# Performance work log

Hardware: AMD Instinct MI355X
Metric: run time of the kernel (lower is better)

Reference implementation:

```python
import jax, jax.numpy as jnp
import numpy as np
import math

D_MODEL = 512
NUM_HEADS = 8
D_HEAD = D_MODEL // NUM_HEADS
B, S = 4, 2048
L = 2 * S - 1  # relative position range


def _rel_shift(pos_score):
    # pos_score: [B, H, S, L] -> [B, H, S, L//2+1] via pad/reshape/slice trick
    b, h, s, l = pos_score.shape
    padded = jnp.pad(pos_score, ((0, 0), (0, 0), (0, 0), (1, 0)))  # [B,H,S,L+1]
    padded = padded.reshape(b, h, l + 1, s)
    shifted = padded[:, :, 1:].reshape(b, h, s, l)
    return shifted[..., : l // 2 + 1]


def setup_inputs() -> dict:
    key = jax.random.key(0)
    ks = jax.random.split(key, 16)
    std = 1.0 / math.sqrt(D_MODEL)
    inp = {
        "query": jax.random.normal(ks[0], (B, S, D_MODEL), jnp.float32),
        "key": jax.random.normal(ks[1], (B, S, D_MODEL), jnp.float32),
        "value": jax.random.normal(ks[2], (B, S, D_MODEL), jnp.float32),
        "pos_embedding": jax.random.normal(ks[3], (B, L, D_MODEL), jnp.float32),
        "Wq": jax.random.normal(ks[4], (D_MODEL, D_MODEL), jnp.float32) * std,
        "bq": jnp.zeros((D_MODEL,), jnp.float32),
        "Wk": jax.random.normal(ks[5], (D_MODEL, D_MODEL), jnp.float32) * std,
        "bk": jnp.zeros((D_MODEL,), jnp.float32),
        "Wv": jax.random.normal(ks[6], (D_MODEL, D_MODEL), jnp.float32) * std,
        "bv": jnp.zeros((D_MODEL,), jnp.float32),
        "Wp": jax.random.normal(ks[7], (D_MODEL, D_MODEL), jnp.float32) * std,
        "u_bias": jax.random.normal(ks[8], (NUM_HEADS, D_HEAD), jnp.float32) * std,
        "v_bias": jax.random.normal(ks[9], (NUM_HEADS, D_HEAD), jnp.float32) * std,
        "Wo": jax.random.normal(ks[10], (D_MODEL, D_MODEL), jnp.float32) * std,
        "bo": jnp.zeros((D_MODEL,), jnp.float32),
    }
    return inp


def reference(query, key, value, pos_embedding, Wq, bq, Wk, bk, Wv, bv, Wp, u_bias, v_bias, Wo, bo):
    b, s, d = query.shape
    h, dh = u_bias.shape
    sqrt_dim = jnp.asarray(math.sqrt(d), query.dtype)

    q = (query @ Wq.T + bq).reshape(b, s, h, dh)
    k = (key @ Wk.T + bk).reshape(b, -1, h, dh)
    v = (value @ Wv.T + bv).reshape(b, -1, h, dh)
    p = (pos_embedding @ Wp.T).reshape(b, -1, h, dh)

    content_score = jnp.einsum("bshd,bthd->bhst", q + u_bias, k)
    pos_score = jnp.einsum("bshd,blhd->bhsl", q + v_bias, p)
    pos_score = _rel_shift(pos_score)  # [B,H,S,S]

    score = (content_score + pos_score) / sqrt_dim
    attn = jax.nn.softmax(score, axis=-1)
    context = jnp.einsum("bhst,bthd->bshd", attn, v).reshape(b, s, d)
    return context @ Wo.T + bo
```

## Files before the change

kernel.cpp:

```cpp
#include <hip/hip_runtime.h>


typedef __bf16 bf16;
typedef __bf16 bf16x4 __attribute__((ext_vector_type(4)));
typedef __bf16 bf16x8 __attribute__((ext_vector_type(8)));
typedef float  f32x4  __attribute__((ext_vector_type(4)));

#define MFMA(A,B,C) __builtin_amdgcn_mfma_f32_16x16x32_bf16((A),(B),(C),0,0,0)

constexpr float SCP = 1.44269504088896f / 22.6274169979695f;

__device__ __forceinline__ void gload16(const void* g, void* l) {
    __builtin_amdgcn_global_load_lds(
        (const __attribute__((address_space(1))) void*)g,
        (__attribute__((address_space(3))) void*)l, 16, 0, 0);
}

constexpr size_t WBYTES   = 512u*512u*2u;
constexpr size_t OFF_WQ   = 0;
constexpr size_t OFF_WK   = OFF_WQ + WBYTES;
constexpr size_t OFF_WV   = OFF_WK + WBYTES;
constexpr size_t OFF_WP   = OFF_WV + WBYTES;
constexpr size_t OFF_WO   = OFF_WP + WBYTES;
constexpr size_t QKV_BYTES = 4ull*8*2048*64*2;
constexpr size_t OFF_QU   = OFF_WO + WBYTES;
constexpr size_t OFF_QV   = OFF_QU + QKV_BYTES;
constexpr size_t OFF_KK   = OFF_QV + QKV_BYTES;
constexpr size_t OFF_VT   = OFF_KK + QKV_BYTES;
constexpr size_t OFF_PP   = OFF_VT + QKV_BYTES;
constexpr size_t PP_BYTES = 4ull*8*4096*64*2;
constexpr size_t OFF_CTX  = OFF_PP + PP_BYTES;

__global__ __launch_bounds__(256) void convert_weights(
    const float* __restrict__ w0, const float* __restrict__ w1,
    const float* __restrict__ w2, const float* __restrict__ w3,
    const float* __restrict__ w4, bf16* __restrict__ dst)
{
    int idx = blockIdx.x * 256 + threadIdx.x;
    const float* srcs[5] = {w0, w1, w2, w3, w4};
    int which = idx >> 15;
    int off   = (idx & 32767) * 8;
    const float* s = srcs[which] + off;
    float4 a = *(const float4*)s;
    float4 b = *(const float4*)(s + 4);
    bf16x8 o;
    o[0]=(bf16)a.x; o[1]=(bf16)a.y; o[2]=(bf16)a.z; o[3]=(bf16)a.w;
    o[4]=(bf16)b.x; o[5]=(bf16)b.y; o[6]=(bf16)b.z; o[7]=(bf16)b.w;
    *(bf16x8*)(dst + (size_t)which * (512*512) + off) = o;
}

template<int MODE>
__global__ __launch_bounds__(256) void gemm_k(
    const void* __restrict__ Av, const bf16* __restrict__ Bw,
    const float* __restrict__ bias, const float* __restrict__ ub,
    const float* __restrict__ vb,
    bf16* __restrict__ o0, bf16* __restrict__ o1, float* __restrict__ of, int M)
{
    __shared__ __align__(16) bf16 As[128 * 64];
    const int tid = threadIdx.x, lane = tid & 63, w = tid >> 6;
    const int r = lane & 15, g = lane >> 4;
    const int m0 = blockIdx.x * 128, n0 = blockIdx.y * 128;
    const int wr = (w >> 1) * 64, wc = (w & 1) * 64;
    f32x4 acc[4][4] = {};

    for (int kt = 0; kt < 512; kt += 64) {
        __syncthreads();
        #pragma unroll
        for (int i = 0; i < 4; i++) {
            int gi = tid + 256 * i;
            int row = gi >> 3, c8 = gi & 7;
            int gm = m0 + row;
            bf16x8 v8;
            if constexpr (MODE == 4) {
                v8 = *(const bf16x8*)((const bf16*)Av + (size_t)gm * 512 + kt + c8 * 8);
            } else {
                float4 a0 = {0,0,0,0}, a1 = {0,0,0,0};
                if (MODE != 3 || gm < M) {
                    const float* ap = (const float*)Av + (size_t)gm * 512 + kt + c8 * 8;
                    a0 = *(const float4*)ap;
                    a1 = *(const float4*)(ap + 4);
                }
                v8[0]=(bf16)a0.x; v8[1]=(bf16)a0.y; v8[2]=(bf16)a0.z; v8[3]=(bf16)a0.w;
                v8[4]=(bf16)a1.x; v8[5]=(bf16)a1.y; v8[6]=(bf16)a1.z; v8[7]=(bf16)a1.w;
            }
            *(bf16x8*)((char*)As + row * 128 + ((c8 ^ (row & 7)) << 4)) = v8;
        }
        __syncthreads();
        #pragma unroll
        for (int ks = 0; ks < 2; ks++) {
            bf16x8 af[4], bfr[4];
            #pragma unroll
            for (int rt = 0; rt < 4; rt++) {
                int row = wr + rt * 16 + r;
                af[rt] = *(const bf16x8*)((const char*)As + row * 128 +
                                          (((ks * 4 + g) ^ (row & 7)) << 4));
            }
            #pragma unroll
            for (int ct = 0; ct < 4; ct++) {
                int n = n0 + wc + ct * 16 + r;
                bfr[ct] = *(const bf16x8*)(Bw + (size_t)n * 512 + kt + ks * 32 + g * 8);
            }
            #pragma unroll
            for (int rt = 0; rt < 4; rt++)
                #pragma unroll
                for (int ct = 0; ct < 4; ct++)
                    acc[rt][ct] = MFMA(af[rt], bfr[ct], acc[rt][ct]);
        }
    }

    #pragma unroll
    for (int rt = 0; rt < 4; rt++) {
        #pragma unroll
        for (int ct = 0; ct < 4; ct++) {
            int gn = n0 + wc + ct * 16 + r;
            int rb = m0 + wr + rt * 16 + g * 4;
            float bsum = (MODE == 3) ? 0.f : bias[gn];
            #pragma unroll
            for (int i = 0; i < 4; i++) {
                int gm = rb + i;
                float val = acc[rt][ct][i];
                if constexpr (MODE == 0) {
                    int b = gm >> 11, s = gm & 2047, h = gn >> 6, dh = gn & 63;
                    size_t o = ((size_t)((b * 8 + h) * 2048 + s)) * 64 + dh;
                    float qb = val + bsum;
                    o0[o] = (bf16)((qb + ub[gn]) * SCP);
                    o1[o] = (bf16)((qb + vb[gn]) * SCP);
                } else if constexpr (MODE == 1) {
                    int b = gm >> 11, s = gm & 2047, h = gn >> 6, dh = gn & 63;
                    o0[((size_t)((b * 8 + h) * 2048 + s)) * 64 +
                       (dh ^ ((s & 7) << 3))] = (bf16)(val + bsum);
                } else if constexpr (MODE == 2) {
                    int b = gm >> 11, s = gm & 2047, h = gn >> 6, dh = gn & 63;
                    int sc = s & 63, sb = s & ~63;
                    o0[((size_t)((b * 8 + h) * 64 + dh)) * 2048 + sb +
                       (sc ^ ((dh & 7) << 3))] = (bf16)(val + bsum);
                } else if constexpr (MODE == 3) {
                    if (gm < M) {
                        int b = gm / 4095, l = gm - b * 4095, h = gn >> 6, dh = gn & 63;
                        o0[((size_t)((b * 8 + h) * 4096 + l)) * 64 + dh] = (bf16)val;
                    }
                } else {
                    of[(size_t)gm * 512 + gn] = val + bsum;
                }
            }
        }
    }
}

__global__ __launch_bounds__(256, 3) void attn_k(
    const bf16* __restrict__ qu, const bf16* __restrict__ qv,
    const bf16* __restrict__ kk, const bf16* __restrict__ vt,
    const bf16* __restrict__ pp, bf16* __restrict__ ctx)
{
    __shared__ __align__(16) bf16 kls[2][64 * 64];
    __shared__ __align__(16) bf16 vls[2][64 * 64];
    __shared__ __align__(16) bf16 ps2[64][80];
    __shared__ __align__(16) bf16 at_t[64 * 64];

    const int lane = threadIdx.x & 63, w = threadIdx.x >> 6;
    const int r = lane & 15, g = lane >> 4;
    const int sw = (r & 7) << 4;
    const int bid = blockIdx.x;
    const int lbid = (bid & 7) * 128 + (bid >> 3);
    const int bh = lbid >> 5;
    const int sigma = lbid & 31;
    const int s0 = sigma * 64;

    const bf16* quB = qu + (size_t)bh * 2048 * 64;
    const bf16* qvB = qv + (size_t)bh * 2048 * 64;
    const bf16* kkB = kk + (size_t)bh * 2048 * 64;
    const bf16* vtB = vt + (size_t)bh * 64 * 2048;
    const bf16* ppB = pp + (size_t)bh * 4096 * 64;

    bf16x8 qaf0, qaf1, qvf0, qvf1;
    {
        const int srow = s0 + 16 * w + r;
        qaf0 = *(const bf16x8*)(quB + (size_t)srow * 64 + g * 8);
        qaf1 = *(const bf16x8*)(quB + (size_t)srow * 64 + 32 + g * 8);
        qvf0 = *(const bf16x8*)(qvB + (size_t)srow * 64 + g * 8);
        qvf1 = *(const bf16x8*)(qvB + (size_t)srow * 64 + 32 + g * 8);
    }
    __builtin_amdgcn_sched_barrier(0);

    bf16* psR = &ps2[16 * w + r][0];
    const int lq = lane >> 3, lc = (lane & 7) << 4;

    bf16x8 pfP[10];
    {
        const int tp = sigma << 6;
        #pragma unroll
        for (int q2 = 0; q2 < 2; q2++) {
            const int ch = 2 * w + q2;
            gload16((const char*)kkB + ((size_t)(tp + ch * 8 + lq) << 7) + lc,
                    (char*)kls[0] + ch * 1024);
            gload16((const char*)vtB + ((size_t)(ch * 8 + lq) << 12) + tp * 2 + lc,
                    (char*)vls[0] + ch * 1024);
        }
        __builtin_amdgcn_sched_barrier(0);
        const int lbw = tp - s0 + 2032 - 16 * w;
        #pragma unroll
        for (int j = 0; j < 5; j++) {
            const bf16* pr = ppB + (size_t)(lbw + j * 16 + r) * 64 + g * 8;
            pfP[2*j]   = *(const bf16x8*)pr;
            pfP[2*j+1] = *(const bf16x8*)(pr + 32);
        }
        __builtin_amdgcn_sched_barrier(0);
    }

    f32x4 oacc[4] = {};
    float sum = 0.f;

    #pragma unroll 2
    for (int n = 0; n < 32; ++n) {
        const int t0 = ((sigma + n) & 31) << 6;
        const int cur = n & 1;
        asm volatile("s_waitcnt vmcnt(10)" ::: "memory");
        __builtin_amdgcn_s_barrier();
        __builtin_amdgcn_sched_barrier(0);

        {
            const int tn = ((sigma + n + 1) & 31) << 6;
            #pragma unroll
            for (int q2 = 0; q2 < 2; q2++) {
                const int ch = 2 * w + q2;
                gload16((const char*)kkB + ((size_t)(tn + ch * 8 + lq) << 7) + lc,
                        (char*)kls[cur ^ 1] + ch * 1024);
                gload16((const char*)vtB + ((size_t)(ch * 8 + lq) << 12) + tn * 2 + lc,
                        (char*)vls[cur ^ 1] + ch * 1024);
            }
        }
        __builtin_amdgcn_sched_barrier(0);

        __builtin_amdgcn_s_setprio(1);
        #pragma unroll
        for (int j = 0; j < 5; j++) {
            f32x4 ps = {};
            ps = MFMA(pfP[2*j],   qvf0, ps);
            ps = MFMA(pfP[2*j+1], qvf1, ps);
            bf16x4 pb;
            pb[0]=(bf16)ps[0]; pb[1]=(bf16)ps[1]; pb[2]=(bf16)ps[2]; pb[3]=(bf16)ps[3];
            *(bf16x4*)(psR + j * 16 + g * 4) = pb;
        }

        f32x4 cc[4];
        #pragma unroll
        for (int c = 0; c < 4; c++) {
            const char* kb = (const char*)kls[cur] + (c * 16 + r) * 128;
            bf16x8 k0 = *(const bf16x8*)(kb + (( 0 + g * 16) ^ sw));
            bf16x8 k1 = *(const bf16x8*)(kb + ((64 + g * 16) ^ sw));
            f32x4 a = {};
            a = MFMA(k0, qaf0, a);
            a = MFMA(k1, qaf1, a);
            cc[c] = a;
        }
        __builtin_amdgcn_s_setprio(0);

        {
            const int tn  = ((sigma + n + 1) & 31) << 6;
            const int lbw = tn - s0 + 2032 - 16 * w;
            #pragma unroll
            for (int j = 0; j < 5; j++) {
                const bf16* pr = ppB + (size_t)(lbw + j * 16 + r) * 64 + g * 8;
                pfP[2*j]   = *(const bf16x8*)pr;
                pfP[2*j+1] = *(const bf16x8*)(pr + 32);
            }
        }

        #pragma unroll
        for (int c = 0; c < 4; c++) {
            const int base = c * 16 + g * 4 + 15 - r;
            float p0 = psR[base], p1 = psR[base+1], p2 = psR[base+2], p3 = psR[base+3];
            float e0 = exp2f(cc[c][0] + p0);
            float e1 = exp2f(cc[c][1] + p1);
            float e2 = exp2f(cc[c][2] + p2);
            float e3 = exp2f(cc[c][3] + p3);
            sum += (e0 + e1) + (e2 + e3);
            bf16x4 pk;
            pk[0]=(bf16)e0; pk[1]=(bf16)e1; pk[2]=(bf16)e2; pk[3]=(bf16)e3;
            *(bf16x4*)((char*)at_t + (16 * w + r) * 128 + ((c * 32 + g * 8) ^ sw)) = pk;
        }

        __builtin_amdgcn_s_setprio(1);
        #pragma unroll
        for (int ks = 0; ks < 2; ks++) {
            bf16x8 af = *(const bf16x8*)((const char*)at_t + (16 * w + r) * 128 +
                                         ((ks * 64 + g * 16) ^ sw));
            #pragma unroll
            for (int nt = 0; nt < 4; nt++) {
                const char* vb_ = (const char*)vls[cur] + (nt * 16 + r) * 128;
                bf16x8 vf = *(const bf16x8*)(vb_ + ((ks * 64 + g * 16) ^ sw));
                oacc[nt] = MFMA(af, vf, oacc[nt]);
            }
        }
        __builtin_amdgcn_s_setprio(0);
    }

    asm volatile("s_waitcnt vmcnt(0)" ::: "memory");

    sum += __shfl_xor(sum, 16);
    sum += __shfl_xor(sum, 32);
    const float inv = 1.f / sum;

    const int b = bh >> 3, h = bh & 7;
    #pragma unroll
    for (int nt = 0; nt < 4; nt++) {
        #pragma unroll
        for (int i = 0; i < 4; i++) {
            const float si = __shfl(inv, g * 4 + i);
            const int s = s0 + 16 * w + g * 4 + i;
            const int col = h * 64 + nt * 16 + r;
            ctx[((size_t)(b * 2048 + s)) * 512 + col] = (bf16)(oacc[nt][i] * si);
        }
    }
}

extern "C" void kernel_launch(void* const* d_in, const int* in_sizes, int n_in,
                              void* d_out, int out_size, void* d_ws, size_t ws_size,
                              hipStream_t stream)
{
    (void)in_sizes; (void)n_in; (void)out_size; (void)ws_size;
    const float* query = (const float*)d_in[0];
    const float* key_  = (const float*)d_in[1];
    const float* value = (const float*)d_in[2];
    const float* pos   = (const float*)d_in[3];
    const float* Wq = (const float*)d_in[4];  const float* bq = (const float*)d_in[5];
    const float* Wk = (const float*)d_in[6];  const float* bk = (const float*)d_in[7];
    const float* Wv = (const float*)d_in[8];  const float* bv = (const float*)d_in[9];
    const float* Wp = (const float*)d_in[10];
    const float* ub = (const float*)d_in[11]; const float* vb = (const float*)d_in[12];
    const float* Wo = (const float*)d_in[13]; const float* bo = (const float*)d_in[14];

    char* ws = (char*)d_ws;
    bf16* Wqb = (bf16*)(ws + OFF_WQ);
    bf16* Wkb = (bf16*)(ws + OFF_WK);
    bf16* Wvb = (bf16*)(ws + OFF_WV);
    bf16* Wpb = (bf16*)(ws + OFF_WP);
    bf16* Wob = (bf16*)(ws + OFF_WO);
    bf16* quP = (bf16*)(ws + OFF_QU);
    bf16* qvP = (bf16*)(ws + OFF_QV);
    bf16* kkP = (bf16*)(ws + OFF_KK);
    bf16* vtP = (bf16*)(ws + OFF_VT);
    bf16* ppP = (bf16*)(ws + OFF_PP);
    bf16* ctxP = (bf16*)(ws + OFF_CTX);

    convert_weights<<<640, 256, 0, stream>>>(Wq, Wk, Wv, Wp, Wo, (bf16*)(ws + OFF_WQ));

    gemm_k<0><<<dim3(64, 4), 256, 0, stream>>>(query, Wqb, bq, ub, vb, quP, qvP, nullptr, 8192);
    gemm_k<1><<<dim3(64, 4), 256, 0, stream>>>(key_,  Wkb, bk, nullptr, nullptr, kkP, nullptr, nullptr, 8192);
    gemm_k<2><<<dim3(64, 4), 256, 0, stream>>>(value, Wvb, bv, nullptr, nullptr, vtP, nullptr, nullptr, 8192);
    gemm_k<3><<<dim3(128, 4), 256, 0, stream>>>(pos,  Wpb, nullptr, nullptr, nullptr, ppP, nullptr, nullptr, 16380);

    attn_k<<<dim3(1024), 256, 0, stream>>>(quP, qvP, kkP, vtP, ppP, ctxP);

    gemm_k<4><<<dim3(64, 4), 256, 0, stream>>>(ctxP, Wob, bo, nullptr, nullptr, nullptr, nullptr, (float*)d_out, 8192);
}
```

Baseline: 303.4 us.

## Double attention query tile to 128 rows per 8-wave block sharing K/V tiles

The attention kernel now runs 512-thread blocks that each cover 128 query rows instead of 64. Each K/V tile staged in LDS is therefore reused by eight waves, so every wave issues half as many async global-to-LDS loads. The grid is halved to match, and the position-score and attention-tile scratch buffers in LDS are enlarged. The s_setprio hints around the MFMA sections are also removed. The cost is a larger LDS footprint and a block-wide barrier over more waves, which may reduce scheduling flexibility.

```diff
diff --git a/kernel.cpp b/kernel.cpp
--- a/kernel.cpp
+++ b/kernel.cpp
@@ -147,24 +147,24 @@
     }
 }
 
-__global__ __launch_bounds__(256, 3) void attn_k(
+__global__ __launch_bounds__(512, 4) void attn_k(
     const bf16* __restrict__ qu, const bf16* __restrict__ qv,
     const bf16* __restrict__ kk, const bf16* __restrict__ vt,
     const bf16* __restrict__ pp, bf16* __restrict__ ctx)
 {
     __shared__ __align__(16) bf16 kls[2][64 * 64];
     __shared__ __align__(16) bf16 vls[2][64 * 64];
-    __shared__ __align__(16) bf16 ps2[64][80];
-    __shared__ __align__(16) bf16 at_t[64 * 64];
+    __shared__ __align__(16) bf16 ps2[128][84];
+    __shared__ __align__(16) bf16 at_t[128 * 64];
 
     const int lane = threadIdx.x & 63, w = threadIdx.x >> 6;
     const int r = lane & 15, g = lane >> 4;
     const int sw = (r & 7) << 4;
     const int bid = blockIdx.x;
-    const int lbid = (bid & 7) * 128 + (bid >> 3);
-    const int bh = lbid >> 5;
-    const int sigma = lbid & 31;
-    const int s0 = sigma * 64;
+    const int lbid = (bid & 7) * 64 + (bid >> 3);
+    const int bh = lbid >> 4;
+    const int sigma = lbid & 15;
+    const int s0 = sigma << 7;
 
     const bf16* quB = qu + (size_t)bh * 2048 * 64;
     const bf16* qvB = qv + (size_t)bh * 2048 * 64;
@@ -187,15 +187,11 @@
 
     bf16x8 pfP[10];
     {
-        const int tp = sigma << 6;
-        #pragma unroll
-        for (int q2 = 0; q2 < 2; q2++) {
-            const int ch = 2 * w + q2;
-            gload16((const char*)kkB + ((size_t)(tp + ch * 8 + lq) << 7) + lc,
-                    (char*)kls[0] + ch * 1024);
-            gload16((const char*)vtB + ((size_t)(ch * 8 + lq) << 12) + tp * 2 + lc,
-                    (char*)vls[0] + ch * 1024);
-        }
+        const int tp = ((sigma * 2) & 31) << 6;
+        gload16((const char*)kkB + ((size_t)(tp + w * 8 + lq) << 7) + lc,
+                (char*)kls[0] + w * 1024);
+        gload16((const char*)vtB + ((size_t)(w * 8 + lq) << 12) + tp * 2 + lc,
+                (char*)vls[0] + w * 1024);
         __builtin_amdgcn_sched_barrier(0);
         const int lbw = tp - s0 + 2032 - 16 * w;
         #pragma unroll
@@ -212,26 +208,20 @@
 
     #pragma unroll 2
     for (int n = 0; n < 32; ++n) {
-        const int t0 = ((sigma + n) & 31) << 6;
         const int cur = n & 1;
         asm volatile("s_waitcnt vmcnt(10)" ::: "memory");
         __builtin_amdgcn_s_barrier();
         __builtin_amdgcn_sched_barrier(0);
 
         {
-            const int tn = ((sigma + n + 1) & 31) << 6;
-            #pragma unroll
-            for (int q2 = 0; q2 < 2; q2++) {
-                const int ch = 2 * w + q2;
-                gload16((const char*)kkB + ((size_t)(tn + ch * 8 + lq) << 7) + lc,
-                        (char*)kls[cur ^ 1] + ch * 1024);
-                gload16((const char*)vtB + ((size_t)(ch * 8 + lq) << 12) + tn * 2 + lc,
-                        (char*)vls[cur ^ 1] + ch * 1024);
-            }
+            const int tn = ((sigma * 2 + n + 1) & 31) << 6;
+            gload16((const char*)kkB + ((size_t)(tn + w * 8 + lq) << 7) + lc,
+                    (char*)kls[cur ^ 1] + w * 1024);
+            gload16((const char*)vtB + ((size_t)(w * 8 + lq) << 12) + tn * 2 + lc,
+                    (char*)vls[cur ^ 1] + w * 1024);
         }
         __builtin_amdgcn_sched_barrier(0);
 
-        __builtin_amdgcn_s_setprio(1);
         #pragma unroll
         for (int j = 0; j < 5; j++) {
             f32x4 ps = {};
@@ -253,10 +243,9 @@
             a = MFMA(k1, qaf1, a);
             cc[c] = a;
         }
-        __builtin_amdgcn_s_setprio(0);
 
         {
-            const int tn  = ((sigma + n + 1) & 31) << 6;
+            const int tn  = ((sigma * 2 + n + 1) & 31) << 6;
             const int lbw = tn - s0 + 2032 - 16 * w;
             #pragma unroll
             for (int j = 0; j < 5; j++) {
@@ -280,7 +269,6 @@
             *(bf16x4*)((char*)at_t + (16 * w + r) * 128 + ((c * 32 + g * 8) ^ sw)) = pk;
         }
 
-        __builtin_amdgcn_s_setprio(1);
         #pragma unroll
         for (int ks = 0; ks < 2; ks++) {
             bf16x8 af = *(const bf16x8*)((const char*)at_t + (16 * w + r) * 128 +
@@ -292,7 +280,6 @@
                 oacc[nt] = MFMA(af, vf, oacc[nt]);
             }
         }
-        __builtin_amdgcn_s_setprio(0);
     }
 
     asm volatile("s_waitcnt vmcnt(0)" ::: "memory");
@@ -350,7 +337,7 @@
     gemm_k<2><<<dim3(64, 4), 256, 0, stream>>>(value, Wvb, bv, nullptr, nullptr, vtP, nullptr, nullptr, 8192);
     gemm_k<3><<<dim3(128, 4), 256, 0, stream>>>(pos,  Wpb, nullptr, nullptr, nullptr, ppP, nullptr, nullptr, 16380);
 
-    attn_k<<<dim3(1024), 256, 0, stream>>>(quP, qvP, kkP, vtP, ppP, ctxP);
+    attn_k<<<dim3(512), 512, 0, stream>>>(quP, qvP, kkP, vtP, ppP, ctxP);
 
     gemm_k<4><<<dim3(64, 4), 256, 0, stream>>>(ctxP, Wob, bo, nullptr, nullptr, nullptr, nullptr, (float*)d_out, 8192);
 }
```

After: 296.2 us. 2.4% less time.
